# Kernel optimization log

Hardware: AMD Instinct MI355X
Metric: run time of the kernel (lower is better)

The kernel has to match this reference:

```python
import jax, jax.numpy as jnp
import numpy as np

N = 100000   # number of points
K = 256      # num_clusters
F = 256      # num_features


def setup_inputs() -> dict:
    key = jax.random.key(0)
    k1, k2 = jax.random.split(key)
    x = jax.random.normal(k1, (1, N, F), dtype=jnp.float32)
    cluster_centers = jax.random.normal(k2, (K, F), dtype=jnp.float32)
    return {"x": x, "cluster_centers": cluster_centers}


def reference(x, cluster_centers):
    # x: (1, n, F); cluster_centers: (K, F)
    # Euclidean distances (1, n, K) via expansion (same math as norm of diff,
    # without materializing the (1, n, K, F) intermediate the torch code builds).
    x_sq = jnp.sum(x * x, axis=-1)                              # (1, n)
    c_sq = jnp.sum(cluster_centers * cluster_centers, axis=-1)  # (K,)
    cross = jnp.einsum('bnf,kf->bnk', x, cluster_centers)       # (1, n, K)
    d2 = x_sq[..., None] + c_sq[None, None, :] - 2.0 * cross
    distances = jnp.sqrt(jnp.maximum(d2, 0.0))                  # (1, n, K)
    # For each cluster, index of the nearest point (argmin over n).
    indices = jnp.argmin(distances, axis=1)                     # (1, K)
    # Gather the features of the nearest point per cluster.
    selected = jnp.take_along_axis(x, indices[:, :, None], axis=1)  # (1, K, F)
    return selected
```

## Files before the change

### kernel.cpp

```cpp
#include <hip/hip_runtime.h>
#include <hip/hip_bf16.h>
#include <stdint.h>

#define N_PTS 100000
#define K_CL  256
#define F_DIM 256

using bf16x8 = __attribute__((ext_vector_type(8))) short;
using f32x4  = __attribute__((ext_vector_type(4))) float;
typedef unsigned long long u64;

__device__ __forceinline__ unsigned pk2(float a, float b) {
    __hip_bfloat162 h = __float22bfloat162_rn(make_float2(a, b));
    unsigned u;
    __builtin_memcpy(&u, &h, 4);
    return u;
}

__global__ void prep_kernel(const float* __restrict__ c,
                            unsigned short* __restrict__ chf,
                            unsigned short* __restrict__ clf,
                            float* __restrict__ csq,
                            u64* __restrict__ best) {
    const int k = blockIdx.x;
    const int lane = threadIdx.x;
    float s = 0.f;
    if (lane < 32) {
        const int b = lane;
        const float* src = c + (size_t)k * F_DIM + b * 8;
        float4 v0 = *(const float4*)(src);
        float4 v1 = *(const float4*)(src + 4);
        float e[8] = {v0.x, v0.y, v0.z, v0.w, v1.x, v1.y, v1.z, v1.w};
        unsigned h[4], l[4];
        #pragma unroll
        for (int j = 0; j < 4; ++j) {
            h[j] = pk2(e[2 * j], e[2 * j + 1]);
            float r0 = e[2 * j]     - __uint_as_float(h[j] << 16);
            float r1 = e[2 * j + 1] - __uint_as_float(h[j] & 0xFFFF0000u);
            l[j] = pk2(r0, r1);
            s = fmaf(e[2 * j], e[2 * j], s);
            s = fmaf(e[2 * j + 1], e[2 * j + 1], s);
        }
        const size_t fi = ((size_t)(k >> 4) * 8 + (b >> 2)) * 64
                        + (b & 3) * 16 + (k & 15);
        *(uint4*)(chf + fi * 8) = make_uint4(h[0], h[1], h[2], h[3]);
        *(uint4*)(clf + fi * 8) = make_uint4(l[0], l[1], l[2], l[3]);
    }
    #pragma unroll
    for (int off = 16; off; off >>= 1) s += __shfl_down(s, off, 64);
    if (lane == 0) { csq[k] = s; best[k] = 0xFFFFFFFFFFFFFFFFULL; }
}

__global__ __launch_bounds__(512, 4)
void cluster_argmin_kernel(const float* __restrict__ x,
                           const unsigned short* __restrict__ chf,
                           const unsigned short* __restrict__ clf,
                           const float* __restrict__ csq,
                           u64* __restrict__ best) {
    __shared__ unsigned short xh_lds[64 * 256];
    __shared__ unsigned short xl_lds[64 * 256];
    __shared__ float xsq_lds[64];

    const int tid  = threadIdx.x;
    const int lane = tid & 63;
    const int w    = __builtin_amdgcn_readfirstlane(tid >> 6);
    const int n0   = blockIdx.x * 64;
    const int r15  = lane & 15;
    const int kg   = lane >> 4;

    float4 v[8];
    #pragma unroll
    for (int i = 0; i < 8; ++i) {
        int gr = n0 + w + i * 8;
        if (gr > N_PTS - 1) gr = N_PTS - 1;
        v[i] = *(const float4*)(x + (size_t)gr * F_DIM + lane * 4);
    }
    #pragma unroll
    for (int i = 0; i < 8; ++i) {
        const int row = w + i * 8;
        float e[4] = {v[i].x, v[i].y, v[i].z, v[i].w};
        unsigned h01 = pk2(e[0], e[1]);
        unsigned h23 = pk2(e[2], e[3]);
        float r0 = e[0] - __uint_as_float(h01 << 16);
        float r1 = e[1] - __uint_as_float(h01 & 0xFFFF0000u);
        float r2 = e[2] - __uint_as_float(h23 << 16);
        float r3 = e[3] - __uint_as_float(h23 & 0xFFFF0000u);
        unsigned l01 = pk2(r0, r1);
        unsigned l23 = pk2(r2, r3);
        const int p = ((lane >> 1) + 2 * row) & 31;
        const int so = row * 256 + p * 8 + (lane & 1) * 4;
        *(uint2*)&xh_lds[so] = make_uint2(h01, h23);
        *(uint2*)&xl_lds[so] = make_uint2(l01, l23);
        float s = fmaf(e[0], e[0], 0.f);
        s = fmaf(e[1], e[1], s);
        s = fmaf(e[2], e[2], s);
        s = fmaf(e[3], e[3], s);
        #pragma unroll
        for (int off = 32; off; off >>= 1) s += __shfl_xor(s, off, 64);
        if (lane == 0) xsq_lds[row] = s;
    }
    __syncthreads();

    const int kb = w * 32;
    const unsigned short* fh0 = chf + ((size_t)(2 * w)     * 8) * 64 * 8 + lane * 8;
    const unsigned short* fh1 = chf + ((size_t)(2 * w + 1) * 8) * 64 * 8 + lane * 8;
    const unsigned short* fl0 = clf + ((size_t)(2 * w)     * 8) * 64 * 8 + lane * 8;
    const unsigned short* fl1 = clf + ((size_t)(2 * w + 1) * 8) * 64 * 8 + lane * 8;

    f32x4 acc[4][2];
    #pragma unroll
    for (int pg = 0; pg < 4; ++pg)
        #pragma unroll
        for (int cg = 0; cg < 2; ++cg)
            acc[pg][cg] = (f32x4){0.f, 0.f, 0.f, 0.f};

    #pragma unroll 2
    for (int it = 0; it < 8; ++it) {
        bf16x8 bh[2], bl[2];
        bh[0] = *(const bf16x8*)(fh0 + (size_t)it * 512);
        bh[1] = *(const bf16x8*)(fh1 + (size_t)it * 512);
        bl[0] = *(const bf16x8*)(fl0 + (size_t)it * 512);
        bl[1] = *(const bf16x8*)(fl1 + (size_t)it * 512);

        bf16x8 xh8[4], xl8[4];
        #pragma unroll
        for (int pg = 0; pg < 4; ++pg) {
            const int row = pg * 16 + r15;
            const int p = (4 * it + kg + 2 * row) & 31;
            const int so = row * 256 + p * 8;
            xh8[pg] = *(const bf16x8*)&xh_lds[so];
            xl8[pg] = *(const bf16x8*)&xl_lds[so];
        }
        __builtin_amdgcn_s_setprio(1);
        #pragma unroll
        for (int pg = 0; pg < 4; ++pg) {
            #pragma unroll
            for (int cg = 0; cg < 2; ++cg) {
                acc[pg][cg] = __builtin_amdgcn_mfma_f32_16x16x32_bf16(
                    xh8[pg], bh[cg], acc[pg][cg], 0, 0, 0);
                acc[pg][cg] = __builtin_amdgcn_mfma_f32_16x16x32_bf16(
                    xh8[pg], bl[cg], acc[pg][cg], 0, 0, 0);
                acc[pg][cg] = __builtin_amdgcn_mfma_f32_16x16x32_bf16(
                    xl8[pg], bh[cg], acc[pg][cg], 0, 0, 0);
            }
        }
        __builtin_amdgcn_s_setprio(0);
    }

    u64 keep = 0xFFFFFFFFFFFFFFFFULL;
    #pragma unroll
    for (int cg = 0; cg < 2; ++cg) {
        const float cs = csq[kb + cg * 16 + r15];
        u64 m = 0xFFFFFFFFFFFFFFFFULL;
        #pragma unroll
        for (int pg = 0; pg < 4; ++pg) {
            #pragma unroll
            for (int r = 0; r < 4; ++r) {
                const int pl = pg * 16 + kg * 4 + r;
                const int n  = n0 + pl;
                float d2 = fmaf(-2.f, acc[pg][cg][r], xsq_lds[pl] + cs);
                d2 = fmaxf(d2, 0.f);
                float d = sqrtf(d2);
                u64 pk = ((u64)__float_as_uint(d) << 32) | (unsigned)n;
                if (n >= N_PTS) pk = 0xFFFFFFFFFFFFFFFFULL;
                m = pk < m ? pk : m;
            }
        }
        u64 o = __shfl_xor(m, 16, 64); m = o < m ? o : m;
        o = __shfl_xor(m, 32, 64);     m = o < m ? o : m;
        if (kg == cg) keep = m;
    }
    if (lane < 32) {
        u64 cur = best[kb + lane];
        if (keep < cur) atomicMin(&best[kb + lane], keep);
    }
}

__global__ void gather_kernel(const float* __restrict__ x,
                              const u64* __restrict__ best,
                              float* __restrict__ out) {
    int k = blockIdx.x;
    unsigned int idx = (unsigned int)(best[k] & 0xFFFFFFFFULL);
    int t = threadIdx.x;
    float4 v = *(const float4*)(x + (size_t)idx * F_DIM + t * 4);
    *(float4*)(out + (size_t)k * F_DIM + t * 4) = v;
}

extern "C" void kernel_launch(void* const* d_in, const int* in_sizes, int n_in,
                              void* d_out, int out_size, void* d_ws, size_t ws_size,
                              hipStream_t stream) {
    const float* x = (const float*)d_in[0];
    const float* c = (const float*)d_in[1];
    float* out = (float*)d_out;

    u64* best  = (u64*)d_ws;
    float* csq = (float*)((char*)d_ws + K_CL * sizeof(u64));

    unsigned short* chf = (unsigned short*)d_out;
    unsigned short* clf = chf + (size_t)K_CL * F_DIM;

    prep_kernel<<<K_CL, 64, 0, stream>>>(c, chf, clf, csq, best);

    int nblocks = (N_PTS + 63) / 64;
    cluster_argmin_kernel<<<nblocks, 512, 0, stream>>>(x, chf, clf, csq, best);

    gather_kernel<<<K_CL, 64, 0, stream>>>(x, best, out);
}
```

Baseline: 190.5 us.

## Make argmin kernel persistent with register-prefetched next tile and wider per-wave cluster tiles

The argmin kernel now launches a fixed grid of 512 blocks of 4 waves that loop over 64-point tiles in a grid-stride fashion. Each wave covers 64 clusters instead of 32. The next tile's x rows are loaded into registers while the current tile's MFMAs and epilogue run, and the norm buffer is double-buffered. The running minimum is kept in registers across tiles, so atomics on the global best array happen once per block rather than once per tile. In exchange, fewer waves are resident per CU, each wave needs more registers for accumulators and prefetched data, and extra block-wide barriers are added.

```diff
diff --git a/kernel.cpp b/kernel.cpp
--- a/kernel.cpp
+++ b/kernel.cpp
@@ -2,9 +2,11 @@
 #include <hip/hip_bf16.h>
 #include <stdint.h>
 
-#define N_PTS 100000
-#define K_CL  256
-#define F_DIM 256
+#define N_PTS  100000
+#define K_CL   256
+#define F_DIM  256
+#define NTILES 1563
+#define GRID   512
 
 using bf16x8 = __attribute__((ext_vector_type(8))) short;
 using f32x4  = __attribute__((ext_vector_type(4))) float;
@@ -51,7 +53,7 @@
     if (lane == 0) { csq[k] = s; best[k] = 0xFFFFFFFFFFFFFFFFULL; }
 }
 
-__global__ __launch_bounds__(512, 4)
+__global__ __launch_bounds__(256, 2)
 void cluster_argmin_kernel(const float* __restrict__ x,
                            const unsigned short* __restrict__ chf,
                            const unsigned short* __restrict__ clf,
@@ -59,121 +61,167 @@
                            u64* __restrict__ best) {
     __shared__ unsigned short xh_lds[64 * 256];
     __shared__ unsigned short xl_lds[64 * 256];
-    __shared__ float xsq_lds[64];
+    __shared__ float xsq_lds[2][64];
 
     const int tid  = threadIdx.x;
     const int lane = tid & 63;
     const int w    = __builtin_amdgcn_readfirstlane(tid >> 6);
-    const int n0   = blockIdx.x * 64;
     const int r15  = lane & 15;
     const int kg   = lane >> 4;
-
-    float4 v[8];
+    const int m    = r15;
+    const int rg   = kg;
+
+    const unsigned short* fh[4];
+    const unsigned short* fl[4];
+    float csq_r[4];
     #pragma unroll
-    for (int i = 0; i < 8; ++i) {
-        int gr = n0 + w + i * 8;
-        if (gr > N_PTS - 1) gr = N_PTS - 1;
-        v[i] = *(const float4*)(x + (size_t)gr * F_DIM + lane * 4);
+    for (int cg = 0; cg < 4; ++cg) {
+        size_t base = (size_t)(4 * w + cg) * 8 * 512 + lane * 8;
+        fh[cg] = chf + base;
+        fl[cg] = clf + base;
+        csq_r[cg] = csq[w * 64 + cg * 16 + r15];
     }
-    #pragma unroll
-    for (int i = 0; i < 8; ++i) {
-        const int row = w + i * 8;
-        float e[4] = {v[i].x, v[i].y, v[i].z, v[i].w};
-        unsigned h01 = pk2(e[0], e[1]);
-        unsigned h23 = pk2(e[2], e[3]);
-        float r0 = e[0] - __uint_as_float(h01 << 16);
-        float r1 = e[1] - __uint_as_float(h01 & 0xFFFF0000u);
-        float r2 = e[2] - __uint_as_float(h23 << 16);
-        float r3 = e[3] - __uint_as_float(h23 & 0xFFFF0000u);
-        unsigned l01 = pk2(r0, r1);
-        unsigned l23 = pk2(r2, r3);
-        const int p = ((lane >> 1) + 2 * row) & 31;
-        const int so = row * 256 + p * 8 + (lane & 1) * 4;
-        *(uint2*)&xh_lds[so] = make_uint2(h01, h23);
-        *(uint2*)&xl_lds[so] = make_uint2(l01, l23);
-        float s = fmaf(e[0], e[0], 0.f);
-        s = fmaf(e[1], e[1], s);
-        s = fmaf(e[2], e[2], s);
-        s = fmaf(e[3], e[3], s);
-        #pragma unroll
-        for (int off = 32; off; off >>= 1) s += __shfl_xor(s, off, 64);
-        if (lane == 0) xsq_lds[row] = s;
+
+    u64 keep = 0xFFFFFFFFFFFFFFFFULL;
+    float4 v[16];
+
+    auto stage_issue = [&](int tile) {
+        const int n0 = tile * 64;
+        #pragma unroll
+        for (int rs = 0; rs < 4; ++rs) {
+            #pragma unroll
+            for (int cs = 0; cs < 4; ++cs) {
+                const int r = rs * 16 + w * 4 + rg;
+                int gn = n0 + r;
+                if (gn > N_PTS - 1) gn = N_PTS - 1;
+                v[rs * 4 + cs] =
+                    *(const float4*)(x + (size_t)gn * F_DIM + cs * 64 + m * 4);
+            }
+        }
+    };
+    auto stage_write = [&](int buf) {
+        #pragma unroll
+        for (int rs = 0; rs < 4; ++rs) {
+            const int r = rs * 16 + w * 4 + rg;
+            float s = 0.f;
+            #pragma unroll
+            for (int cs = 0; cs < 4; ++cs) {
+                float4 e = v[rs * 4 + cs];
+                unsigned h01 = pk2(e.x, e.y);
+                unsigned h23 = pk2(e.z, e.w);
+                float q0 = e.x - __uint_as_float(h01 << 16);
+                float q1 = e.y - __uint_as_float(h01 & 0xFFFF0000u);
+                float q2 = e.z - __uint_as_float(h23 << 16);
+                float q3 = e.w - __uint_as_float(h23 & 0xFFFF0000u);
+                unsigned l01 = pk2(q0, q1);
+                unsigned l23 = pk2(q2, q3);
+                const int b = cs * 8 + (m >> 1);
+                const int p = (b + 9 * r + 2 * (r >> 4)) & 31;
+                const int so = r * 256 + p * 8 + (m & 1) * 4;
+                *(uint2*)&xh_lds[so] = make_uint2(h01, h23);
+                *(uint2*)&xl_lds[so] = make_uint2(l01, l23);
+                s = fmaf(e.x, e.x, s);
+                s = fmaf(e.y, e.y, s);
+                s = fmaf(e.z, e.z, s);
+                s = fmaf(e.w, e.w, s);
+            }
+            s += __shfl_xor(s, 1, 64);
+            s += __shfl_xor(s, 2, 64);
+            s += __shfl_xor(s, 4, 64);
+            s += __shfl_xor(s, 8, 64);
+            if (m == 0) xsq_lds[buf][r] = s;
+        }
+    };
+
+    int tile = blockIdx.x;
+    stage_issue(tile);
+    stage_write(0);
+    __syncthreads();
+    int buf = 0;
+
+    while (true) {
+        const int nxt = tile + GRID;
+        const bool have_nxt = (nxt < NTILES);
+        const int n0 = tile * 64;
+
+        f32x4 acc[4][4];
+        #pragma unroll
+        for (int pg = 0; pg < 4; ++pg)
+            #pragma unroll
+            for (int cg = 0; cg < 4; ++cg)
+                acc[pg][cg] = (f32x4){0.f, 0.f, 0.f, 0.f};
+
+        #pragma unroll 2
+        for (int it = 0; it < 8; ++it) {
+            bf16x8 bh[4], bl[4];
+            #pragma unroll
+            for (int cg = 0; cg < 4; ++cg) {
+                bh[cg] = *(const bf16x8*)(fh[cg] + it * 512);
+                bl[cg] = *(const bf16x8*)(fl[cg] + it * 512);
+            }
+            bf16x8 xh8[4], xl8[4];
+            #pragma unroll
+            for (int pg = 0; pg < 4; ++pg) {
+                const int r = pg * 16 + r15;
+                const int p = (4 * it + kg + 9 * r + 2 * (r >> 4)) & 31;
+                const int so = r * 256 + p * 8;
+                xh8[pg] = *(const bf16x8*)&xh_lds[so];
+                xl8[pg] = *(const bf16x8*)&xl_lds[so];
+            }
+            __builtin_amdgcn_s_setprio(1);
+            #pragma unroll
+            for (int pg = 0; pg < 4; ++pg) {
+                #pragma unroll
+                for (int cg = 0; cg < 4; ++cg) {
+                    acc[pg][cg] = __builtin_amdgcn_mfma_f32_16x16x32_bf16(
+                        xh8[pg], bh[cg], acc[pg][cg], 0, 0, 0);
+                    acc[pg][cg] = __builtin_amdgcn_mfma_f32_16x16x32_bf16(
+                        xh8[pg], bl[cg], acc[pg][cg], 0, 0, 0);
+                    acc[pg][cg] = __builtin_amdgcn_mfma_f32_16x16x32_bf16(
+                        xl8[pg], bh[cg], acc[pg][cg], 0, 0, 0);
+                }
+            }
+            __builtin_amdgcn_s_setprio(0);
+        }
+
+        if (have_nxt) stage_issue(nxt);
+
+        float4 xs[4];
+        #pragma unroll
+        for (int pg = 0; pg < 4; ++pg)
+            xs[pg] = *(const float4*)&xsq_lds[buf][pg * 16 + kg * 4];
+        #pragma unroll
+        for (int cg = 0; cg < 4; ++cg) {
+            const float cs = csq_r[cg];
+            u64 mm = 0xFFFFFFFFFFFFFFFFULL;
+            #pragma unroll
+            for (int pg = 0; pg < 4; ++pg) {
+                #pragma unroll
+                for (int rr = 0; rr < 4; ++rr) {
+                    const int n = n0 + pg * 16 + kg * 4 + rr;
+                    float d2 = fmaf(-2.f, acc[pg][cg][rr], xs[pg][rr] + cs);
+                    d2 = fmaxf(d2, 0.f);
+                    float d = sqrtf(d2);
+                    u64 pk = ((u64)__float_as_uint(d) << 32) | (unsigned)n;
+                    if (n >= N_PTS) pk = 0xFFFFFFFFFFFFFFFFULL;
+                    mm = pk < mm ? pk : mm;
+                }
+            }
+            u64 o = __shfl_xor(mm, 16, 64); mm = o < mm ? o : mm;
+            o = __shfl_xor(mm, 32, 64);     mm = o < mm ? o : mm;
+            if (kg == cg) keep = keep < mm ? keep : mm;
+        }
+
+        __syncthreads();
+        if (have_nxt) stage_write(buf ^ 1);
+        __syncthreads();
+        if (!have_nxt) break;
+        tile = nxt;
+        buf ^= 1;
     }
-    __syncthreads();
-
-    const int kb = w * 32;
-    const unsigned short* fh0 = chf + ((size_t)(2 * w)     * 8) * 64 * 8 + lane * 8;
-    const unsigned short* fh1 = chf + ((size_t)(2 * w + 1) * 8) * 64 * 8 + lane * 8;
-    const unsigned short* fl0 = clf + ((size_t)(2 * w)     * 8) * 64 * 8 + lane * 8;
-    const unsigned short* fl1 = clf + ((size_t)(2 * w + 1) * 8) * 64 * 8 + lane * 8;
-
-    f32x4 acc[4][2];
-    #pragma unroll
-    for (int pg = 0; pg < 4; ++pg)
-        #pragma unroll
-        for (int cg = 0; cg < 2; ++cg)
-            acc[pg][cg] = (f32x4){0.f, 0.f, 0.f, 0.f};
-
-    #pragma unroll 2
-    for (int it = 0; it < 8; ++it) {
-        bf16x8 bh[2], bl[2];
-        bh[0] = *(const bf16x8*)(fh0 + (size_t)it * 512);
-        bh[1] = *(const bf16x8*)(fh1 + (size_t)it * 512);
-        bl[0] = *(const bf16x8*)(fl0 + (size_t)it * 512);
-        bl[1] = *(const bf16x8*)(fl1 + (size_t)it * 512);
-
-        bf16x8 xh8[4], xl8[4];
-        #pragma unroll
-        for (int pg = 0; pg < 4; ++pg) {
-            const int row = pg * 16 + r15;
-            const int p = (4 * it + kg + 2 * row) & 31;
-            const int so = row * 256 + p * 8;
-            xh8[pg] = *(const bf16x8*)&xh_lds[so];
-            xl8[pg] = *(const bf16x8*)&xl_lds[so];
-        }
-        __builtin_amdgcn_s_setprio(1);
-        #pragma unroll
-        for (int pg = 0; pg < 4; ++pg) {
-            #pragma unroll
-            for (int cg = 0; cg < 2; ++cg) {
-                acc[pg][cg] = __builtin_amdgcn_mfma_f32_16x16x32_bf16(
-                    xh8[pg], bh[cg], acc[pg][cg], 0, 0, 0);
-                acc[pg][cg] = __builtin_amdgcn_mfma_f32_16x16x32_bf16(
-                    xh8[pg], bl[cg], acc[pg][cg], 0, 0, 0);
-                acc[pg][cg] = __builtin_amdgcn_mfma_f32_16x16x32_bf16(
-                    xl8[pg], bh[cg], acc[pg][cg], 0, 0, 0);
-            }
-        }
-        __builtin_amdgcn_s_setprio(0);
-    }
-
-    u64 keep = 0xFFFFFFFFFFFFFFFFULL;
-    #pragma unroll
-    for (int cg = 0; cg < 2; ++cg) {
-        const float cs = csq[kb + cg * 16 + r15];
-        u64 m = 0xFFFFFFFFFFFFFFFFULL;
-        #pragma unroll
-        for (int pg = 0; pg < 4; ++pg) {
-            #pragma unroll
-            for (int r = 0; r < 4; ++r) {
-                const int pl = pg * 16 + kg * 4 + r;
-                const int n  = n0 + pl;
-                float d2 = fmaf(-2.f, acc[pg][cg][r], xsq_lds[pl] + cs);
-                d2 = fmaxf(d2, 0.f);
-                float d = sqrtf(d2);
-                u64 pk = ((u64)__float_as_uint(d) << 32) | (unsigned)n;
-                if (n >= N_PTS) pk = 0xFFFFFFFFFFFFFFFFULL;
-                m = pk < m ? pk : m;
-            }
-        }
-        u64 o = __shfl_xor(m, 16, 64); m = o < m ? o : m;
-        o = __shfl_xor(m, 32, 64);     m = o < m ? o : m;
-        if (kg == cg) keep = m;
-    }
-    if (lane < 32) {
-        u64 cur = best[kb + lane];
-        if (keep < cur) atomicMin(&best[kb + lane], keep);
-    }
+
+    u64 cur = best[w * 64 + lane];
+    if (keep < cur) atomicMin(&best[w * 64 + lane], keep);
 }
 
 __global__ void gather_kernel(const float* __restrict__ x,
@@ -201,8 +249,7 @@
 
     prep_kernel<<<K_CL, 64, 0, stream>>>(c, chf, clf, csq, best);
 
-    int nblocks = (N_PTS + 63) / 64;
-    cluster_argmin_kernel<<<nblocks, 512, 0, stream>>>(x, chf, clf, csq, best);
+    cluster_argmin_kernel<<<GRID, 256, 0, stream>>>(x, chf, clf, csq, best);
 
     gather_kernel<<<K_CL, 64, 0, stream>>>(x, best, out);
 }
```

After: 205.3 us. +7.8%, slower.

## Make argmin kernel persistent with register-prefetched next tile and fewer atomics

Applied to the files above, without the earlier changes.

Replaces the one-block-per-64-point-tile launch with a persistent grid of 256 blocks that loop over tiles. The next tile's x rows are loaded into registers during the current tile's MFMA work, then staged into LDS with a new XOR swizzle. The per-cluster running minimum stays in registers, so atomics happen once per block instead of once per tile. It also double-buffers the center-fragment global loads, compares squared distances before a single sqrt per lane, and lowers the launch-bounds occupancy hint. The cost is more register pressure and only 256 blocks, which on a GPU with many CUs may leave some CUs underfilled and lose latency hiding.

```diff
diff --git a/kernel.cpp b/kernel.cpp
--- a/kernel.cpp
+++ b/kernel.cpp
@@ -2,9 +2,11 @@
 #include <hip/hip_bf16.h>
 #include <stdint.h>
 
-#define N_PTS 100000
-#define K_CL  256
-#define F_DIM 256
+#define N_PTS  100000
+#define K_CL   256
+#define F_DIM  256
+#define NTILES 1563
+#define GRID   256
 
 using bf16x8 = __attribute__((ext_vector_type(8))) short;
 using f32x4  = __attribute__((ext_vector_type(4))) float;
@@ -51,7 +53,7 @@
     if (lane == 0) { csq[k] = s; best[k] = 0xFFFFFFFFFFFFFFFFULL; }
 }
 
-__global__ __launch_bounds__(512, 4)
+__global__ __launch_bounds__(512, 2)
 void cluster_argmin_kernel(const float* __restrict__ x,
                            const unsigned short* __restrict__ chf,
                            const unsigned short* __restrict__ clf,
@@ -64,115 +66,168 @@
     const int tid  = threadIdx.x;
     const int lane = tid & 63;
     const int w    = __builtin_amdgcn_readfirstlane(tid >> 6);
-    const int n0   = blockIdx.x * 64;
     const int r15  = lane & 15;
     const int kg   = lane >> 4;
-
+    const int srow = tid >> 3;
+    const int sl   = tid & 7;
+
+    const unsigned short* fh0 = chf + (size_t)(2 * w)     * 8 * 512 + lane * 8;
+    const unsigned short* fh1 = chf + (size_t)(2 * w + 1) * 8 * 512 + lane * 8;
+    const unsigned short* fl0 = clf + (size_t)(2 * w)     * 8 * 512 + lane * 8;
+    const unsigned short* fl1 = clf + (size_t)(2 * w + 1) * 8 * 512 + lane * 8;
+    const float csq0 = csq[w * 32 + r15];
+    const float csq1 = csq[w * 32 + 16 + r15];
+
+    u64 keep = 0xFFFFFFFFFFFFFFFFULL;
     float4 v[8];
-    #pragma unroll
-    for (int i = 0; i < 8; ++i) {
-        int gr = n0 + w + i * 8;
+
+    auto load_v = [&](int t) {
+        int gr = t * 64 + srow;
         if (gr > N_PTS - 1) gr = N_PTS - 1;
-        v[i] = *(const float4*)(x + (size_t)gr * F_DIM + lane * 4);
+        const float* base = x + (size_t)gr * F_DIM + sl * 8;
+        #pragma unroll
+        for (int j = 0; j < 4; ++j) {
+            v[2 * j]     = *(const float4*)(base + j * 64);
+            v[2 * j + 1] = *(const float4*)(base + j * 64 + 4);
+        }
+    };
+    auto write_stage = [&]() {
+        float s = 0.f;
+        #pragma unroll
+        for (int j = 0; j < 4; ++j) {
+            float4 a = v[2 * j], b = v[2 * j + 1];
+            unsigned h0 = pk2(a.x, a.y), h1 = pk2(a.z, a.w);
+            unsigned h2 = pk2(b.x, b.y), h3 = pk2(b.z, b.w);
+            float q0 = a.x - __uint_as_float(h0 << 16);
+            float q1 = a.y - __uint_as_float(h0 & 0xFFFF0000u);
+            float q2 = a.z - __uint_as_float(h1 << 16);
+            float q3 = a.w - __uint_as_float(h1 & 0xFFFF0000u);
+            float q4 = b.x - __uint_as_float(h2 << 16);
+            float q5 = b.y - __uint_as_float(h2 & 0xFFFF0000u);
+            float q6 = b.z - __uint_as_float(h3 << 16);
+            float q7 = b.w - __uint_as_float(h3 & 0xFFFF0000u);
+            unsigned l0 = pk2(q0, q1), l1 = pk2(q2, q3);
+            unsigned l2 = pk2(q4, q5), l3 = pk2(q6, q7);
+            const int blk = sl + 8 * j;
+            const int p   = blk ^ ((srow & 7) << 2);
+            const int so  = srow * 256 + p * 8;
+            *(uint4*)&xh_lds[so] = make_uint4(h0, h1, h2, h3);
+            *(uint4*)&xl_lds[so] = make_uint4(l0, l1, l2, l3);
+            s = fmaf(a.x, a.x, s); s = fmaf(a.y, a.y, s);
+            s = fmaf(a.z, a.z, s); s = fmaf(a.w, a.w, s);
+            s = fmaf(b.x, b.x, s); s = fmaf(b.y, b.y, s);
+            s = fmaf(b.z, b.z, s); s = fmaf(b.w, b.w, s);
+        }
+        s += __shfl_xor(s, 1, 64);
+        s += __shfl_xor(s, 2, 64);
+        s += __shfl_xor(s, 4, 64);
+        if (sl == 0) xsq_lds[srow] = s;
+    };
+
+    int tile = blockIdx.x;
+    load_v(tile);
+    write_stage();
+    __syncthreads();
+
+    while (true) {
+        const int nxt = tile + GRID;
+        const bool have = (nxt < NTILES);
+        if (have) load_v(nxt);
+
+        f32x4 acc[4][2];
+        #pragma unroll
+        for (int pg = 0; pg < 4; ++pg) {
+            acc[pg][0] = (f32x4){0.f, 0.f, 0.f, 0.f};
+            acc[pg][1] = (f32x4){0.f, 0.f, 0.f, 0.f};
+        }
+
+        auto compute_it = [&](int it, bf16x8 bh0, bf16x8 bh1,
+                              bf16x8 bl0, bf16x8 bl1) {
+            bf16x8 xh8[4], xl8[4];
+            const int p = ((it ^ (r15 & 7)) << 2) | kg;
+            #pragma unroll
+            for (int pg = 0; pg < 4; ++pg) {
+                const int so = (pg * 16 + r15) * 256 + p * 8;
+                xh8[pg] = *(const bf16x8*)&xh_lds[so];
+                xl8[pg] = *(const bf16x8*)&xl_lds[so];
+            }
+            __builtin_amdgcn_s_setprio(1);
+            #pragma unroll
+            for (int pg = 0; pg < 4; ++pg) {
+                acc[pg][0] = __builtin_amdgcn_mfma_f32_16x16x32_bf16(
+                    xh8[pg], bh0, acc[pg][0], 0, 0, 0);
+                acc[pg][0] = __builtin_amdgcn_mfma_f32_16x16x32_bf16(
+                    xh8[pg], bl0, acc[pg][0], 0, 0, 0);
+                acc[pg][0] = __builtin_amdgcn_mfma_f32_16x16x32_bf16(
+                    xl8[pg], bh0, acc[pg][0], 0, 0, 0);
+                acc[pg][1] = __builtin_amdgcn_mfma_f32_16x16x32_bf16(
+                    xh8[pg], bh1, acc[pg][1], 0, 0, 0);
+                acc[pg][1] = __builtin_amdgcn_mfma_f32_16x16x32_bf16(
+                    xh8[pg], bl1, acc[pg][1], 0, 0, 0);
+                acc[pg][1] = __builtin_amdgcn_mfma_f32_16x16x32_bf16(
+                    xl8[pg], bh1, acc[pg][1], 0, 0, 0);
+            }
+            __builtin_amdgcn_s_setprio(0);
+        };
+
+        bf16x8 bBh0 = *(const bf16x8*)(fh0), bBh1 = *(const bf16x8*)(fh1);
+        bf16x8 bBl0 = *(const bf16x8*)(fl0), bBl1 = *(const bf16x8*)(fl1);
+        #pragma unroll
+        for (int ii = 0; ii < 4; ++ii) {
+            const int itE = 2 * ii, itO = 2 * ii + 1;
+            bf16x8 bAh0 = *(const bf16x8*)(fh0 + itO * 512);
+            bf16x8 bAh1 = *(const bf16x8*)(fh1 + itO * 512);
+            bf16x8 bAl0 = *(const bf16x8*)(fl0 + itO * 512);
+            bf16x8 bAl1 = *(const bf16x8*)(fl1 + itO * 512);
+            compute_it(itE, bBh0, bBh1, bBl0, bBl1);
+            if (ii < 3) {
+                bBh0 = *(const bf16x8*)(fh0 + (itE + 2) * 512);
+                bBh1 = *(const bf16x8*)(fh1 + (itE + 2) * 512);
+                bBl0 = *(const bf16x8*)(fl0 + (itE + 2) * 512);
+                bBl1 = *(const bf16x8*)(fl1 + (itE + 2) * 512);
+            }
+            compute_it(itO, bAh0, bAh1, bAl0, bAl1);
+        }
+
+        const int n0t = tile * 64;
+        float4 xs[4];
+        #pragma unroll
+        for (int pg = 0; pg < 4; ++pg)
+            xs[pg] = *(const float4*)&xsq_lds[pg * 16 + kg * 4];
+        #pragma unroll
+        for (int cg = 0; cg < 2; ++cg) {
+            const float cs = (cg == 0) ? csq0 : csq1;
+            float bd2 = 3.4e38f;
+            int bn = 0;
+            #pragma unroll
+            for (int pg = 0; pg < 4; ++pg) {
+                #pragma unroll
+                for (int rr = 0; rr < 4; ++rr) {
+                    const int n = n0t + pg * 16 + kg * 4 + rr;
+                    float d2 = fmaf(-2.f, acc[pg][cg][rr], xs[pg][rr] + cs);
+                    bool ok = (n < N_PTS) && (d2 < bd2);
+                    bd2 = ok ? d2 : bd2;
+                    bn  = ok ? n  : bn;
+                }
+            }
+            float d = sqrtf(fmaxf(bd2, 0.f));
+            u64 pk = ((u64)__float_as_uint(d) << 32) | (unsigned)bn;
+            u64 o = __shfl_xor(pk, 16, 64); pk = o < pk ? o : pk;
+            o = __shfl_xor(pk, 32, 64);     pk = o < pk ? o : pk;
+            if (kg == cg) keep = pk < keep ? pk : keep;
+        }
+
+        __syncthreads();
+        if (have) write_stage();
+        __syncthreads();
+        if (!have) break;
+        tile = nxt;
     }
-    #pragma unroll
-    for (int i = 0; i < 8; ++i) {
-        const int row = w + i * 8;
-        float e[4] = {v[i].x, v[i].y, v[i].z, v[i].w};
-        unsigned h01 = pk2(e[0], e[1]);
-        unsigned h23 = pk2(e[2], e[3]);
-        float r0 = e[0] - __uint_as_float(h01 << 16);
-        float r1 = e[1] - __uint_as_float(h01 & 0xFFFF0000u);
-        float r2 = e[2] - __uint_as_float(h23 << 16);
-        float r3 = e[3] - __uint_as_float(h23 & 0xFFFF0000u);
-        unsigned l01 = pk2(r0, r1);
-        unsigned l23 = pk2(r2, r3);
-        const int p = ((lane >> 1) + 2 * row) & 31;
-        const int so = row * 256 + p * 8 + (lane & 1) * 4;
-        *(uint2*)&xh_lds[so] = make_uint2(h01, h23);
-        *(uint2*)&xl_lds[so] = make_uint2(l01, l23);
-        float s = fmaf(e[0], e[0], 0.f);
-        s = fmaf(e[1], e[1], s);
-        s = fmaf(e[2], e[2], s);
-        s = fmaf(e[3], e[3], s);
-        #pragma unroll
-        for (int off = 32; off; off >>= 1) s += __shfl_xor(s, off, 64);
-        if (lane == 0) xsq_lds[row] = s;
-    }
-    __syncthreads();
-
-    const int kb = w * 32;
-    const unsigned short* fh0 = chf + ((size_t)(2 * w)     * 8) * 64 * 8 + lane * 8;
-    const unsigned short* fh1 = chf + ((size_t)(2 * w + 1) * 8) * 64 * 8 + lane * 8;
-    const unsigned short* fl0 = clf + ((size_t)(2 * w)     * 8) * 64 * 8 + lane * 8;
-    const unsigned short* fl1 = clf + ((size_t)(2 * w + 1) * 8) * 64 * 8 + lane * 8;
-
-    f32x4 acc[4][2];
-    #pragma unroll
-    for (int pg = 0; pg < 4; ++pg)
-        #pragma unroll
-        for (int cg = 0; cg < 2; ++cg)
-            acc[pg][cg] = (f32x4){0.f, 0.f, 0.f, 0.f};
-
-    #pragma unroll 2
-    for (int it = 0; it < 8; ++it) {
-        bf16x8 bh[2], bl[2];
-        bh[0] = *(const bf16x8*)(fh0 + (size_t)it * 512);
-        bh[1] = *(const bf16x8*)(fh1 + (size_t)it * 512);
-        bl[0] = *(const bf16x8*)(fl0 + (size_t)it * 512);
-        bl[1] = *(const bf16x8*)(fl1 + (size_t)it * 512);
-
-        bf16x8 xh8[4], xl8[4];
-        #pragma unroll
-        for (int pg = 0; pg < 4; ++pg) {
-            const int row = pg * 16 + r15;
-            const int p = (4 * it + kg + 2 * row) & 31;
-            const int so = row * 256 + p * 8;
-            xh8[pg] = *(const bf16x8*)&xh_lds[so];
-            xl8[pg] = *(const bf16x8*)&xl_lds[so];
-        }
-        __builtin_amdgcn_s_setprio(1);
-        #pragma unroll
-        for (int pg = 0; pg < 4; ++pg) {
-            #pragma unroll
-            for (int cg = 0; cg < 2; ++cg) {
-                acc[pg][cg] = __builtin_amdgcn_mfma_f32_16x16x32_bf16(
-                    xh8[pg], bh[cg], acc[pg][cg], 0, 0, 0);
-                acc[pg][cg] = __builtin_amdgcn_mfma_f32_16x16x32_bf16(
-                    xh8[pg], bl[cg], acc[pg][cg], 0, 0, 0);
-                acc[pg][cg] = __builtin_amdgcn_mfma_f32_16x16x32_bf16(
-                    xl8[pg], bh[cg], acc[pg][cg], 0, 0, 0);
-            }
-        }
-        __builtin_amdgcn_s_setprio(0);
-    }
-
-    u64 keep = 0xFFFFFFFFFFFFFFFFULL;
-    #pragma unroll
-    for (int cg = 0; cg < 2; ++cg) {
-        const float cs = csq[kb + cg * 16 + r15];
-        u64 m = 0xFFFFFFFFFFFFFFFFULL;
-        #pragma unroll
-        for (int pg = 0; pg < 4; ++pg) {
-            #pragma unroll
-            for (int r = 0; r < 4; ++r) {
-                const int pl = pg * 16 + kg * 4 + r;
-                const int n  = n0 + pl;
-                float d2 = fmaf(-2.f, acc[pg][cg][r], xsq_lds[pl] + cs);
-                d2 = fmaxf(d2, 0.f);
-                float d = sqrtf(d2);
-                u64 pk = ((u64)__float_as_uint(d) << 32) | (unsigned)n;
-                if (n >= N_PTS) pk = 0xFFFFFFFFFFFFFFFFULL;
-                m = pk < m ? pk : m;
-            }
-        }
-        u64 o = __shfl_xor(m, 16, 64); m = o < m ? o : m;
-        o = __shfl_xor(m, 32, 64);     m = o < m ? o : m;
-        if (kg == cg) keep = m;
-    }
+
     if (lane < 32) {
-        u64 cur = best[kb + lane];
-        if (keep < cur) atomicMin(&best[kb + lane], keep);
+        const int cl_ = w * 32 + lane;
+        u64 cur = best[cl_];
+        if (keep < cur) atomicMin(&best[cl_], keep);
     }
 }
 
@@ -201,8 +256,7 @@
 
     prep_kernel<<<K_CL, 64, 0, stream>>>(c, chf, clf, csq, best);
 
-    int nblocks = (N_PTS + 63) / 64;
-    cluster_argmin_kernel<<<nblocks, 512, 0, stream>>>(x, chf, clf, csq, best);
+    cluster_argmin_kernel<<<GRID, 512, 0, stream>>>(x, chf, clf, csq, best);
 
     gather_kernel<<<K_CL, 64, 0, stream>>>(x, best, out);
 }
```

After: 199.3 us. +4.6%, slower.
